# Optimization experiments

Hardware: AMD Instinct MI355X
Metric: run time of the kernel (lower is better)

The kernel has to match this reference:

```python
import jax, jax.numpy as jnp
import numpy as np

N, IN_F, H, D = 4096, 256, 4, 64  # nodes, in_features, num_heads, head_dim
NEG_BIG = -9e15


def setup_inputs() -> dict:
    key = jax.random.key(0)
    k1, k2, k3, k4, k5 = jax.random.split(key, 5)
    x = jax.random.normal(k1, (N, IN_F), dtype=jnp.float32)
    adj = jax.random.randint(k2, (N, N), 0, 2, dtype=jnp.int32)
    # xavier-uniform-scale init for W: [in_features, H*D]
    lim_w = float(np.sqrt(6.0 / (IN_F + H * D)))
    W = jax.random.uniform(k3, (IN_F, H * D), minval=-lim_w, maxval=lim_w, dtype=jnp.float32)
    # a: [2*D, 1] split into a1 (dest half) and a2 (source half)
    lim_a = float(np.sqrt(6.0 / (2 * D + 1)))
    a1 = jax.random.uniform(k4, (D,), minval=-lim_a, maxval=lim_a, dtype=jnp.float32)
    a2 = jax.random.uniform(k5, (D,), minval=-lim_a, maxval=lim_a, dtype=jnp.float32)
    return {"x": x, "adj": adj, "W": W, "a1": a1, "a2": a2}


def reference(x, adj, W, a1, a2):
    n = x.shape[0]
    h = (x @ W).reshape(n, H, D)                      # [N, H, D]
    # e[i,j,h] = leaky_relu(<h_i, a1> + <h_j, a2>)  (== concat([h_i,h_j]) @ a)
    si = jnp.einsum("nhd,d->nh", h, a1)               # [N, H]
    sj = jnp.einsum("nhd,d->nh", h, a2)               # [N, H]
    e = jax.nn.leaky_relu(si[:, None, :] + sj[None, :, :], negative_slope=0.2)
    e = jnp.where(adj[:, :, None] > 0, e, NEG_BIG)    # mask non-edges
    att = jax.nn.softmax(e, axis=1)                   # softmax over neighbors j
    out = jnp.einsum("ijh,jhd->ihd", att, h)          # per-head aggregation
    return out.reshape(n, H * D)                      # concat heads
```

## Files before the change

kernel.cpp:

```cpp
#include <hip/hip_runtime.h>
#include <hip/hip_bf16.h>


typedef __bf16 bf16x8 __attribute__((ext_vector_type(8)));
typedef __bf16 bf16x4 __attribute__((ext_vector_type(4)));
typedef float floatx4 __attribute__((ext_vector_type(4)));

#define LOG2E 1.4426950408889634f
#define NN 4096

__device__ __forceinline__ void gl16(const void* g, void* l) {
  __builtin_amdgcn_global_load_lds(
      (const __attribute__((address_space(1))) unsigned int*)g,
      (__attribute__((address_space(3))) unsigned int*)l, 16, 0, 0);
}

__global__ __launch_bounds__(256) void gat_pack(
    const int* __restrict__ adj, const float* __restrict__ x,
    const float* __restrict__ W, unsigned short* __restrict__ adjm,
    __bf16* __restrict__ xb, __bf16* __restrict__ WT) {
  __shared__ __align__(16) int buf[4096];
  const int b = blockIdx.x, t = threadIdx.x;
  const int w = t >> 6, lane = t & 63;

  if (b < 2048) {
    for (int s = 0; s < 2; ++s) {
      const int row = b * 2 + s;
      const int* sp = adj + (size_t)row * 4096 + w * 1024 + lane * 4;
      int* dp = buf + w * 1024 + lane * 4;
#pragma unroll
      for (int r = 0; r < 4; ++r) gl16(sp + r * 256, dp + r * 256);
      __syncthreads();
      const int4* rp = (const int4*)(buf + t * 16);
      int4 v0 = rp[0], v1 = rp[1], v2 = rp[2], v3 = rp[3];
      int vs[16] = {v0.x, v0.y, v0.z, v0.w, v1.x, v1.y, v1.z, v1.w,
                    v2.x, v2.y, v2.z, v2.w, v3.x, v3.y, v3.z, v3.w};
      unsigned int m = 0;
#pragma unroll
      for (int q = 0; q < 16; ++q) m |= (vs[q] != 0) ? (1u << q) : 0u;
      adjm[(size_t)row * 256 + t] = (unsigned short)m;
      __syncthreads();
    }
    return;
  }

  if (b < 2064) {
    const int k0 = (b - 2048) * 16;
    const float* sp = W + (size_t)k0 * 256 + w * 1024 + lane * 4;
    int* dp = buf + w * 1024 + lane * 4;
#pragma unroll
    for (int r = 0; r < 4; ++r) gl16(sp + r * 256, dp + r * 256);
    __syncthreads();
    const float* wl = (const float*)buf;
    bf16x8 o0, o1;
#pragma unroll
    for (int k = 0; k < 8; ++k) o0[k] = (__bf16)wl[k * 256 + t];
#pragma unroll
    for (int k = 0; k < 8; ++k) o1[k] = (__bf16)wl[(8 + k) * 256 + t];
    __bf16* op = WT + (size_t)t * 256 + k0;
    *(bf16x8*)op = o0;
    *(bf16x8*)(op + 8) = o1;
    return;
  }

  const int bi = b - 2064;
  const float4* x4 = (const float4*)x;
#pragma unroll
  for (int it = 0; it < 4; ++it) {
    int g = it * 65536 + bi * 256 + t;
    float4 f = x4[g];
    bf16x4 o = {(__bf16)f.x, (__bf16)f.y, (__bf16)f.z, (__bf16)f.w};
    *(bf16x4*)(xb + (size_t)g * 4) = o;
  }
}

__global__ __launch_bounds__(256, 2) void gat_prep(
    const __bf16* __restrict__ xb, const __bf16* __restrict__ WT,
    const float* __restrict__ a1, const float* __restrict__ a2,
    __bf16* __restrict__ hTf, float* __restrict__ siT, float2* __restrict__ vv2T,
    float* __restrict__ sjm) {
  __shared__ __align__(16) char plds[65536];
  const int b = blockIdx.x, t = threadIdx.x;
  const int it = b & 63, hh = b >> 6;
  const int i0 = it * 64, c0 = hh * 64;
  const int w = t >> 6, lane = t & 63, quad = lane >> 4, l16 = lane & 15;

  const __bf16* asrc = xb + ((size_t)(i0 + w * 16 + l16) << 8) + quad * 8;
  const __bf16* bsrc = WT + ((size_t)(c0 + w * 16 + l16) << 8) + quad * 8;
#pragma unroll
  for (int kw = 0; kw < 8; ++kw) {
    gl16(asrc + kw * 32, plds + (((w * 8 + kw) << 10) + (lane << 4)));
    gl16(bsrc + kw * 32, plds + 32768 + (((w * 8 + kw) << 10) + (lane << 4)));
  }

  float a1v[4], a2v[4];
#pragma unroll
  for (int nt = 0; nt < 4; ++nt) {
    a1v[nt] = a1[nt * 16 + l16];
    a2v[nt] = a2[nt * 16 + l16];
  }
  __syncthreads();

  floatx4 zv = {0.f, 0.f, 0.f, 0.f};
  floatx4 acc[4] = {zv, zv, zv, zv};
#pragma unroll
  for (int kw = 0; kw < 8; ++kw) {
    bf16x8 af = *(const bf16x8*)(plds + (((w * 8 + kw) << 10) + (lane << 4)));
#pragma unroll
    for (int nt = 0; nt < 4; ++nt) {
      bf16x8 bfr = *(const bf16x8*)(plds + 32768 + (((nt * 8 + kw) << 10) + (lane << 4)));
      acc[nt] = __builtin_amdgcn_mfma_f32_16x16x32_bf16(af, bfr, acc[nt], 0, 0, 0);
    }
  }
  __syncthreads();

  float* hl = (float*)plds;
  float* sjb = (float*)(plds + 20480);
#pragma unroll
  for (int reg = 0; reg < 4; ++reg) {
    const int row = w * 16 + quad * 4 + reg;
#pragma unroll
    for (int nt = 0; nt < 4; ++nt) hl[row * 68 + nt * 16 + l16] = acc[nt][reg];
    float s1 = acc[0][reg] * a1v[0] + acc[1][reg] * a1v[1] +
               acc[2][reg] * a1v[2] + acc[3][reg] * a1v[3];
    float s2 = acc[0][reg] * a2v[0] + acc[1][reg] * a2v[1] +
               acc[2][reg] * a2v[2] + acc[3][reg] * a2v[3];
#pragma unroll
    for (int off = 1; off < 16; off <<= 1) {
      s1 += __shfl_xor(s1, off);
      s2 += __shfl_xor(s2, off);
    }
    if (l16 == 0) {
      siT[hh * NN + i0 + row] = s1 * LOG2E;
      float sjs = s2 * LOG2E;
      vv2T[hh * NN + i0 + row] =
          make_float2(__builtin_amdgcn_exp2f(sjs), __builtin_amdgcn_exp2f(0.2f * sjs));
      sjb[row] = sjs;
    }
  }
  __syncthreads();

  if (t < 64) {
    float v = sjb[t];
#pragma unroll
    for (int off = 1; off < 64; off <<= 1) v = fmaxf(v, __shfl_xor(v, off));
    if (t == 0) sjm[it * 4 + hh] = v;
  }

  const int nt2 = t >> 6;
#pragma unroll
  for (int ch = 0; ch < 2; ++ch) {
    bf16x8 h0;
#pragma unroll
    for (int jj = 0; jj < 8; ++jj)
      h0[jj] = (__bf16)hl[(ch * 32 + quad * 8 + jj) * 68 + nt2 * 16 + l16];
    *(bf16x8*)((char*)hTf +
               ((((size_t)hh * 128 + it * 2 + ch) * 4 + nt2) << 10) + (lane << 4)) = h0;
  }
}

__global__ __launch_bounds__(256, 2) void gat_attn(
    const __bf16* __restrict__ hTf, const float* __restrict__ siT,
    const float2* __restrict__ vv2T, const float* __restrict__ sjm,
    const unsigned int* __restrict__ adjw,
    float* __restrict__ pacc, float* __restrict__ pl) {
  __shared__ __align__(16) char lds[65536];
  const int t = threadIdx.x;
  const int w = t >> 6, lane = t & 63, quad = lane >> 4, l16 = lane & 15;
  const int i0 = blockIdx.x * 64, hh = blockIdx.y, s = blockIdx.z;
  const int jbeg = s * 2048;

  const char* hsrc = (const char*)hTf +
      (((size_t)hh * 128 + (jbeg >> 5) + w * 2) << 12) + (lane << 4);
  const float2* vw = vv2T + (size_t)hh * NN + jbeg + w * 64;

  const unsigned int* mp[4];
#pragma unroll
  for (int mt = 0; mt < 4; ++mt)
    mp[mt] = adjw + (size_t)(i0 + mt * 16 + l16) * 128 + (jbeg >> 5) + w * 2;

  uint2 mc[4], mn[4];
  float4 qc[2][4], qn[2][4];
#pragma unroll
  for (int mt = 0; mt < 4; ++mt) mc[mt] = *(const uint2*)mp[mt];
#pragma unroll
  for (int k = 0; k < 2; ++k) {
    const float4* qp = (const float4*)(vw + k * 32 + quad * 8);
#pragma unroll
    for (int c = 0; c < 4; ++c) qc[k][c] = qp[c];
  }
#pragma unroll
  for (int k = 0; k < 2; ++k)
#pragma unroll
    for (int nt = 0; nt < 4; ++nt)
      gl16(hsrc + ((k * 4 + nt) << 10),
           lds + (((w * 8 + k * 4 + nt) << 10) + (lane << 4)));

  float vv = sjm[lane * 4 + hh];
#pragma unroll
  for (int off = 1; off < 64; off <<= 1) vv = fmaxf(vv, __shfl_xor(vv, off));
  float u[4], u2[4];
#pragma unroll
  for (int mt = 0; mt < 4; ++mt) {
    float sis = siT[hh * NN + i0 + mt * 16 + l16];
    float tt = sis + vv;
    float m = fmaxf(tt, 0.2f * tt);
    u[mt] = __builtin_amdgcn_exp2f(sis - m);
    u2[mt] = __builtin_amdgcn_exp2f(0.2f * sis - m);
  }

  bf16x8 ones;
#pragma unroll
  for (int ii = 0; ii < 8; ++ii) ones[ii] = (__bf16)1.0f;

  floatx4 zv = {0.f, 0.f, 0.f, 0.f};
  floatx4 acc[4][4], lacc[4];
#pragma unroll
  for (int mt = 0; mt < 4; ++mt) {
    lacc[mt] = zv;
#pragma unroll
    for (int nt = 0; nt < 4; ++nt) acc[mt][nt] = zv;
  }

  __syncthreads();

  for (int win = 0; win < 8; ++win) {
    const int p = win & 1;
    const char* hb = lds + p * 32768;

    if (win + 1 < 8) {
#pragma unroll
      for (int mt = 0; mt < 4; ++mt)
        mn[mt] = *(const uint2*)(mp[mt] + (win + 1) * 8);
#pragma unroll
      for (int k = 0; k < 2; ++k) {
        const float4* qp = (const float4*)(vw + (win + 1) * 256 + k * 32 + quad * 8);
#pragma unroll
        for (int c = 0; c < 4; ++c) qn[k][c] = qp[c];
      }
      char* hbn = lds + (p ^ 1) * 32768;
      const char* hs = hsrc + (win + 1) * 32768;
#pragma unroll
      for (int k = 0; k < 2; ++k)
#pragma unroll
        for (int nt = 0; nt < 4; ++nt)
          gl16(hs + ((k * 4 + nt) << 10),
               hbn + (((w * 8 + k * 4 + nt) << 10) + (lane << 4)));
    }

#pragma unroll
    for (int k = 0; k < 2; ++k) {
      bf16x8 bfr[4];
#pragma unroll
      for (int nt = 0; nt < 4; ++nt)
        bfr[nt] = *(const bf16x8*)(hb + ((w * 8 + k * 4 + nt) << 10) + (lane << 4));
#pragma unroll
      for (int mt = 0; mt < 4; ++mt) {
        unsigned int m8 = (k ? mc[mt].y : mc[mt].x) >> (quad * 8);
        bf16x8 af;
#pragma unroll
        for (int c = 0; c < 4; ++c) {
          float p0 = fmaxf(u[mt] * qc[k][c].x, u2[mt] * qc[k][c].y);
          float p1 = fmaxf(u[mt] * qc[k][c].z, u2[mt] * qc[k][c].w);
          int b0 = ((int)(m8 << (31 - 2 * c))) >> 31;
          int b1 = ((int)(m8 << (30 - 2 * c))) >> 31;
          af[2 * c]     = (__bf16)__uint_as_float(__float_as_uint(p0) & (unsigned)b0);
          af[2 * c + 1] = (__bf16)__uint_as_float(__float_as_uint(p1) & (unsigned)b1);
        }
#pragma unroll
        for (int nt = 0; nt < 4; ++nt)
          acc[mt][nt] = __builtin_amdgcn_mfma_f32_16x16x32_bf16(af, bfr[nt],
                                                                acc[mt][nt], 0, 0, 0);
        lacc[mt] = __builtin_amdgcn_mfma_f32_16x16x32_bf16(af, ones, lacc[mt], 0, 0, 0);
      }
    }
#pragma unroll
    for (int mt = 0; mt < 4; ++mt) mc[mt] = mn[mt];
#pragma unroll
    for (int k = 0; k < 2; ++k)
#pragma unroll
      for (int c = 0; c < 4; ++c) qc[k][c] = qn[k][c];
    __syncthreads();
  }

  float* accs = (float*)lds;
  float* lsum = (float*)(lds + 34816);
  if (w < 2) {
#pragma unroll
    for (int mt = 0; mt < 4; ++mt)
#pragma unroll
      for (int reg = 0; reg < 4; ++reg) {
        int row = mt * 16 + quad * 4 + reg;
        float* ap = accs + (w * 64 + row) * 68;
#pragma unroll
        for (int nt = 0; nt < 4; ++nt)
          ap[nt * 16 + l16] = acc[mt][nt][reg];
        if (l16 == 0) lsum[w * 64 + row] = lacc[mt][reg];
      }
  }
  __syncthreads();
  if (w >= 2) {
    const int bb = w - 2;
#pragma unroll
    for (int mt = 0; mt < 4; ++mt)
#pragma unroll
      for (int reg = 0; reg < 4; ++reg) {
        int row = mt * 16 + quad * 4 + reg;
        float* ap = accs + (bb * 64 + row) * 68;
#pragma unroll
        for (int nt = 0; nt < 4; ++nt)
          ap[nt * 16 + l16] += acc[mt][nt][reg];
        if (l16 == 0) lsum[bb * 64 + row] += lacc[mt][reg];
      }
  }
  __syncthreads();

  const int r = t >> 2, cb = (t & 3) * 16;
  float* op = pacc + (size_t)s * NN * 256 + (size_t)(i0 + r) * 256 + hh * 64 + cb;
#pragma unroll
  for (int c4 = 0; c4 < 4; ++c4) {
    int c = cb + c4 * 4;
    float4 o;
    o.x = accs[r * 68 + c + 0] + accs[(64 + r) * 68 + c + 0];
    o.y = accs[r * 68 + c + 1] + accs[(64 + r) * 68 + c + 1];
    o.z = accs[r * 68 + c + 2] + accs[(64 + r) * 68 + c + 2];
    o.w = accs[r * 68 + c + 3] + accs[(64 + r) * 68 + c + 3];
    *(float4*)(op + c4 * 4) = o;
  }
  if (t < 64)
    pl[(size_t)s * NN * 4 + (i0 + t) * 4 + hh] = lsum[t] + lsum[64 + t];
}

__global__ __launch_bounds__(256) void gat_reduce(
    const float* __restrict__ pacc, const float* __restrict__ pl,
    float* __restrict__ out) {
  const int e4 = blockIdx.x * 256 + threadIdx.x;
  const int e = e4 * 4;
  const int i = e >> 8;
  const int h = (e & 255) >> 6;
  float4 a0 = *(const float4*)(pacc + e);
  float4 a1 = *(const float4*)(pacc + (size_t)NN * 256 + e);
  float l = pl[i * 4 + h] + pl[(size_t)NN * 4 + i * 4 + h];
  float inv = 1.0f / l;
  *(float4*)(out + e) = make_float4((a0.x + a1.x) * inv, (a0.y + a1.y) * inv,
                                    (a0.z + a1.z) * inv, (a0.w + a1.w) * inv);
}

extern "C" void kernel_launch(void* const* d_in, const int* in_sizes, int n_in,
                              void* d_out, int out_size, void* d_ws, size_t ws_size,
                              hipStream_t stream) {
  const float* x  = (const float*)d_in[0];
  const int*   adj = (const int*)d_in[1];
  const float* W  = (const float*)d_in[2];
  const float* a1 = (const float*)d_in[3];
  const float* a2 = (const float*)d_in[4];
  float* out = (float*)d_out;
  char* ws = (char*)d_ws;

  __bf16* hTf  = (__bf16*)ws;
  float*  siT  = (float*)(ws + 2097152);
  float2* vv2T = (float2*)(ws + 2162688);
  float*  sjm  = (float*)(ws + 2293760);
  unsigned short* adjb = (unsigned short*)(ws + 2297856);
  __bf16* xb   = (__bf16*)(ws + 4395008);
  __bf16* WT   = (__bf16*)(ws + 6492160);
  float*  pacc = (float*)(ws + 6623232);
  float*  pl   = (float*)(ws + 15011840);

  gat_pack<<<2320, 256, 0, stream>>>(adj, x, W, adjb, xb, WT);
  gat_prep<<<256, 256, 0, stream>>>(xb, WT, a1, a2, hTf, siT, vv2T, sjm);
  gat_attn<<<dim3(64, 4, 2), 256, 0, stream>>>(hTf, siT, vv2T, sjm,
                                               (const unsigned int*)adjb, pacc, pl);
  gat_reduce<<<1024, 256, 0, stream>>>(pacc, pl, out);
}
```

Before: 141.3 us.

## Drop split-K in attention kernel, shrink row tile, and fuse normalization

The attention kernel no longer splits the neighbor dimension into two halves written to partial buffers. Each block now covers 32 rows over all 4096 neighbors and divides by the row sum directly, which removes the separate reduce kernel and the partial-sum round trip through global memory. The adjacency pack kernel also moves from two rows per block to one row per block, doubling its block count. In exchange each block now runs twice as many sequential windows, and the H tiles are reloaded by twice as many row blocks.

After: 141.4 us. About the same (+0.1%).

```diff
diff --git a/kernel.cpp b/kernel.cpp
--- a/kernel.cpp
+++ b/kernel.cpp
@@ -23,29 +23,25 @@
   const int b = blockIdx.x, t = threadIdx.x;
   const int w = t >> 6, lane = t & 63;
 
-  if (b < 2048) {
-    for (int s = 0; s < 2; ++s) {
-      const int row = b * 2 + s;
-      const int* sp = adj + (size_t)row * 4096 + w * 1024 + lane * 4;
-      int* dp = buf + w * 1024 + lane * 4;
-#pragma unroll
-      for (int r = 0; r < 4; ++r) gl16(sp + r * 256, dp + r * 256);
-      __syncthreads();
-      const int4* rp = (const int4*)(buf + t * 16);
-      int4 v0 = rp[0], v1 = rp[1], v2 = rp[2], v3 = rp[3];
-      int vs[16] = {v0.x, v0.y, v0.z, v0.w, v1.x, v1.y, v1.z, v1.w,
-                    v2.x, v2.y, v2.z, v2.w, v3.x, v3.y, v3.z, v3.w};
-      unsigned int m = 0;
-#pragma unroll
-      for (int q = 0; q < 16; ++q) m |= (vs[q] != 0) ? (1u << q) : 0u;
-      adjm[(size_t)row * 256 + t] = (unsigned short)m;
-      __syncthreads();
-    }
+  if (b < 4096) {
+    const int* sp = adj + (size_t)b * 4096 + w * 1024 + lane * 4;
+    int* dp = buf + w * 1024 + lane * 4;
+#pragma unroll
+    for (int r = 0; r < 4; ++r) gl16(sp + r * 256, dp + r * 256);
+    __syncthreads();
+    const int4* rp = (const int4*)(buf + t * 16);
+    int4 v0 = rp[0], v1 = rp[1], v2 = rp[2], v3 = rp[3];
+    int vs[16] = {v0.x, v0.y, v0.z, v0.w, v1.x, v1.y, v1.z, v1.w,
+                  v2.x, v2.y, v2.z, v2.w, v3.x, v3.y, v3.z, v3.w};
+    unsigned int m = 0;
+#pragma unroll
+    for (int q = 0; q < 16; ++q) m |= (vs[q] != 0) ? (1u << q) : 0u;
+    adjm[(size_t)b * 256 + t] = (unsigned short)m;
     return;
   }
 
-  if (b < 2064) {
-    const int k0 = (b - 2048) * 16;
+  if (b < 4112) {
+    const int k0 = (b - 4096) * 16;
     const float* sp = W + (size_t)k0 * 256 + w * 1024 + lane * 4;
     int* dp = buf + w * 1024 + lane * 4;
 #pragma unroll
@@ -63,7 +59,7 @@
     return;
   }
 
-  const int bi = b - 2064;
+  const int bi = b - 4112;
   const float4* x4 = (const float4*)x;
 #pragma unroll
   for (int it = 0; it < 4; ++it) {
@@ -162,27 +158,24 @@
 __global__ __launch_bounds__(256, 2) void gat_attn(
     const __bf16* __restrict__ hTf, const float* __restrict__ siT,
     const float2* __restrict__ vv2T, const float* __restrict__ sjm,
-    const unsigned int* __restrict__ adjw,
-    float* __restrict__ pacc, float* __restrict__ pl) {
+    const unsigned int* __restrict__ adjw, float* __restrict__ out) {
   __shared__ __align__(16) char lds[65536];
   const int t = threadIdx.x;
   const int w = t >> 6, lane = t & 63, quad = lane >> 4, l16 = lane & 15;
-  const int i0 = blockIdx.x * 64, hh = blockIdx.y, s = blockIdx.z;
-  const int jbeg = s * 2048;
-
-  const char* hsrc = (const char*)hTf +
-      (((size_t)hh * 128 + (jbeg >> 5) + w * 2) << 12) + (lane << 4);
-  const float2* vw = vv2T + (size_t)hh * NN + jbeg + w * 64;
-
-  const unsigned int* mp[4];
-#pragma unroll
-  for (int mt = 0; mt < 4; ++mt)
-    mp[mt] = adjw + (size_t)(i0 + mt * 16 + l16) * 128 + (jbeg >> 5) + w * 2;
-
-  uint2 mc[4], mn[4];
+  const int i0 = blockIdx.x * 32, hh = blockIdx.y;
+
+  const char* hsrc = (const char*)hTf + (((size_t)hh * 128 + w * 2) << 12) + (lane << 4);
+  const float2* vw = vv2T + (size_t)hh * NN + w * 64;
+
+  const unsigned int* mp[2];
+#pragma unroll
+  for (int mt = 0; mt < 2; ++mt)
+    mp[mt] = adjw + (size_t)(i0 + mt * 16 + l16) * 128 + w * 2;
+
+  uint2 mc[2], mn[2];
   float4 qc[2][4], qn[2][4];
 #pragma unroll
-  for (int mt = 0; mt < 4; ++mt) mc[mt] = *(const uint2*)mp[mt];
+  for (int mt = 0; mt < 2; ++mt) mc[mt] = *(const uint2*)mp[mt];
 #pragma unroll
   for (int k = 0; k < 2; ++k) {
     const float4* qp = (const float4*)(vw + k * 32 + quad * 8);
@@ -199,9 +192,9 @@
   float vv = sjm[lane * 4 + hh];
 #pragma unroll
   for (int off = 1; off < 64; off <<= 1) vv = fmaxf(vv, __shfl_xor(vv, off));
-  float u[4], u2[4];
-#pragma unroll
-  for (int mt = 0; mt < 4; ++mt) {
+  float u[2], u2[2];
+#pragma unroll
+  for (int mt = 0; mt < 2; ++mt) {
     float sis = siT[hh * NN + i0 + mt * 16 + l16];
     float tt = sis + vv;
     float m = fmaxf(tt, 0.2f * tt);
@@ -214,9 +207,9 @@
   for (int ii = 0; ii < 8; ++ii) ones[ii] = (__bf16)1.0f;
 
   floatx4 zv = {0.f, 0.f, 0.f, 0.f};
-  floatx4 acc[4][4], lacc[4];
-#pragma unroll
-  for (int mt = 0; mt < 4; ++mt) {
+  floatx4 acc[2][4], lacc[2];
+#pragma unroll
+  for (int mt = 0; mt < 2; ++mt) {
     lacc[mt] = zv;
 #pragma unroll
     for (int nt = 0; nt < 4; ++nt) acc[mt][nt] = zv;
@@ -224,13 +217,13 @@
 
   __syncthreads();
 
-  for (int win = 0; win < 8; ++win) {
+  for (int win = 0; win < 16; ++win) {
     const int p = win & 1;
     const char* hb = lds + p * 32768;
 
-    if (win + 1 < 8) {
-#pragma unroll
-      for (int mt = 0; mt < 4; ++mt)
+    if (win + 1 < 16) {
+#pragma unroll
+      for (int mt = 0; mt < 2; ++mt)
         mn[mt] = *(const uint2*)(mp[mt] + (win + 1) * 8);
 #pragma unroll
       for (int k = 0; k < 2; ++k) {
@@ -255,7 +248,7 @@
       for (int nt = 0; nt < 4; ++nt)
         bfr[nt] = *(const bf16x8*)(hb + ((w * 8 + k * 4 + nt) << 10) + (lane << 4));
 #pragma unroll
-      for (int mt = 0; mt < 4; ++mt) {
+      for (int mt = 0; mt < 2; ++mt) {
         unsigned int m8 = (k ? mc[mt].y : mc[mt].x) >> (quad * 8);
         bf16x8 af;
 #pragma unroll
@@ -275,7 +268,7 @@
       }
     }
 #pragma unroll
-    for (int mt = 0; mt < 4; ++mt) mc[mt] = mn[mt];
+    for (int mt = 0; mt < 2; ++mt) mc[mt] = mn[mt];
 #pragma unroll
     for (int k = 0; k < 2; ++k)
 #pragma unroll
@@ -284,66 +277,47 @@
   }
 
   float* accs = (float*)lds;
-  float* lsum = (float*)(lds + 34816);
+  float* lsum = (float*)(lds + 17408);
   if (w < 2) {
 #pragma unroll
-    for (int mt = 0; mt < 4; ++mt)
+    for (int mt = 0; mt < 2; ++mt)
 #pragma unroll
       for (int reg = 0; reg < 4; ++reg) {
         int row = mt * 16 + quad * 4 + reg;
-        float* ap = accs + (w * 64 + row) * 68;
+        float* ap = accs + (w * 32 + row) * 68;
 #pragma unroll
         for (int nt = 0; nt < 4; ++nt)
           ap[nt * 16 + l16] = acc[mt][nt][reg];
-        if (l16 == 0) lsum[w * 64 + row] = lacc[mt][reg];
+        if (l16 == 0) lsum[w * 32 + row] = lacc[mt][reg];
       }
   }
   __syncthreads();
   if (w >= 2) {
     const int bb = w - 2;
 #pragma unroll
-    for (int mt = 0; mt < 4; ++mt)
+    for (int mt = 0; mt < 2; ++mt)
 #pragma unroll
       for (int reg = 0; reg < 4; ++reg) {
         int row = mt * 16 + quad * 4 + reg;
-        float* ap = accs + (bb * 64 + row) * 68;
+        float* ap = accs + (bb * 32 + row) * 68;
 #pragma unroll
         for (int nt = 0; nt < 4; ++nt)
           ap[nt * 16 + l16] += acc[mt][nt][reg];
-        if (l16 == 0) lsum[bb * 64 + row] += lacc[mt][reg];
+        if (l16 == 0) lsum[bb * 32 + row] += lacc[mt][reg];
       }
   }
   __syncthreads();
 
-  const int r = t >> 2, cb = (t & 3) * 16;
-  float* op = pacc + (size_t)s * NN * 256 + (size_t)(i0 + r) * 256 + hh * 64 + cb;
-#pragma unroll
-  for (int c4 = 0; c4 < 4; ++c4) {
-    int c = cb + c4 * 4;
-    float4 o;
-    o.x = accs[r * 68 + c + 0] + accs[(64 + r) * 68 + c + 0];
-    o.y = accs[r * 68 + c + 1] + accs[(64 + r) * 68 + c + 1];
-    o.z = accs[r * 68 + c + 2] + accs[(64 + r) * 68 + c + 2];
-    o.w = accs[r * 68 + c + 3] + accs[(64 + r) * 68 + c + 3];
-    *(float4*)(op + c4 * 4) = o;
-  }
-  if (t < 64)
-    pl[(size_t)s * NN * 4 + (i0 + t) * 4 + hh] = lsum[t] + lsum[64 + t];
-}
-
-__global__ __launch_bounds__(256) void gat_reduce(
-    const float* __restrict__ pacc, const float* __restrict__ pl,
-    float* __restrict__ out) {
-  const int e4 = blockIdx.x * 256 + threadIdx.x;
-  const int e = e4 * 4;
-  const int i = e >> 8;
-  const int h = (e & 255) >> 6;
-  float4 a0 = *(const float4*)(pacc + e);
-  float4 a1 = *(const float4*)(pacc + (size_t)NN * 256 + e);
-  float l = pl[i * 4 + h] + pl[(size_t)NN * 4 + i * 4 + h];
+  const int r = t >> 3, c = (t & 7) * 8;
+  float l = lsum[r] + lsum[32 + r];
   float inv = 1.0f / l;
-  *(float4*)(out + e) = make_float4((a0.x + a1.x) * inv, (a0.y + a1.y) * inv,
-                                    (a0.z + a1.z) * inv, (a0.w + a1.w) * inv);
+  float o[8];
+#pragma unroll
+  for (int k = 0; k < 8; ++k)
+    o[k] = (accs[r * 68 + c + k] + accs[(32 + r) * 68 + c + k]) * inv;
+  float* op = out + (size_t)(i0 + r) * 256 + hh * 64 + c;
+  *(float4*)op = make_float4(o[0], o[1], o[2], o[3]);
+  *(float4*)(op + 4) = make_float4(o[4], o[5], o[6], o[7]);
 }
 
 extern "C" void kernel_launch(void* const* d_in, const int* in_sizes, int n_in,
@@ -364,12 +338,9 @@
   unsigned short* adjb = (unsigned short*)(ws + 2297856);
   __bf16* xb   = (__bf16*)(ws + 4395008);
   __bf16* WT   = (__bf16*)(ws + 6492160);
-  float*  pacc = (float*)(ws + 6623232);
-  float*  pl   = (float*)(ws + 15011840);
-
-  gat_pack<<<2320, 256, 0, stream>>>(adj, x, W, adjb, xb, WT);
+
+  gat_pack<<<4368, 256, 0, stream>>>(adj, x, W, adjb, xb, WT);
   gat_prep<<<256, 256, 0, stream>>>(xb, WT, a1, a2, hTf, siT, vv2T, sjm);
-  gat_attn<<<dim3(64, 4, 2), 256, 0, stream>>>(hTf, siT, vv2T, sjm,
-                                               (const unsigned int*)adjb, pacc, pl);
-  gat_reduce<<<1024, 256, 0, stream>>>(pacc, pl, out);
-}
+  gat_attn<<<dim3(128, 4), 256, 0, stream>>>(hTf, siT, vv2T, sjm,
+                                             (const unsigned int*)adjb, out);
+}
```
